# Kernel tuning notes

Hardware: AMD Instinct MI355X
Metric: run time of the kernel (lower is better)

The kernel has to match this reference:

```python
import jax, jax.numpy as jnp
import numpy as np

NUM_HEADS = 16
ROPE_BASE = 10000.0
QK_GAIN_INIT = 12.0
EPS = 1e-6
# head_config = alternating ['rope','nope',...]; 1.0 -> RoPE applied to this head
ROPE_MASK = jnp.asarray(np.tile([1.0, 0.0], NUM_HEADS // 2), dtype=jnp.float32)


def setup_inputs() -> dict:
    key = jax.random.key(0)
    k0, k1, k2 = jax.random.split(key, 3)
    B, S, Dm = 2, 2048, 2048
    x = jax.random.normal(k0, (B, S, Dm), dtype=jnp.float32)
    # fused QKV projection and output projection (out_proj flagged zero-init in the
    # original; we use small random init so outputs/grads are non-trivial)
    w_qkv = jax.random.normal(k1, (Dm, 3 * Dm), dtype=jnp.float32) * (Dm ** -0.5)
    w_out = jax.random.normal(k2, (Dm, Dm), dtype=jnp.float32) * (Dm ** -0.5)
    q_gain = jnp.full((NUM_HEADS,), QK_GAIN_INIT, dtype=jnp.float32)
    return {"x": x, "w_qkv": w_qkv, "w_out": w_out, "q_gain": q_gain}


def _rope_cos_sin(seqlen, head_dim, dtype):
    half = head_dim // 2
    inv_freq = ROPE_BASE ** (-jnp.arange(0, half, dtype=jnp.float32) / half)
    theta = jnp.arange(seqlen, dtype=jnp.float32)[:, None] * inv_freq[None, :]  # [S, D/2]
    return jnp.cos(theta).astype(dtype), jnp.sin(theta).astype(dtype)


def _apply_rope(t, cos, sin):
    # t: [B, S, H, D]; cos/sin: [S, D/2] -> broadcast [1, S, 1, D/2]
    d2 = t.shape[-1] // 2
    t1, t2 = t[..., :d2], t[..., d2:]
    c = cos[None, :, None, :]
    s = sin[None, :, None, :]
    return jnp.concatenate([t1 * c - t2 * s, t1 * s + t2 * c], axis=-1)


def _unit_norm(t):
    # per-head-dim L2 normalization (qk-norm)
    return t * jax.lax.rsqrt(jnp.sum(t * t, axis=-1, keepdims=True) + EPS)


def reference(x, w_qkv, w_out, q_gain):
    B, S, Dm = x.shape
    H = NUM_HEADS
    D = Dm // H
    qkv = (x @ w_qkv).reshape(B, S, 3, H, D)
    q, k, v = qkv[:, :, 0], qkv[:, :, 1], qkv[:, :, 2]  # [B, S, H, D]
    q = _unit_norm(q)
    k = _unit_norm(k)
    cos, sin = _rope_cos_sin(S, D, x.dtype)
    m = ROPE_MASK[None, None, :, None]  # heterogeneous per-head dispatch
    q = m * _apply_rope(q, cos, sin) + (1.0 - m) * q
    k = m * _apply_rope(k, cos, sin) + (1.0 - m) * k
    # per-head learned qk gain instead of 1/sqrt(d)
    logits = jnp.einsum('bshd,bthd->bhst', q, k) * q_gain[None, :, None, None]
    causal = jnp.tril(jnp.ones((S, S), dtype=bool))
    logits = jnp.where(causal[None, None], logits, jnp.finfo(logits.dtype).min)
    attn = jax.nn.softmax(logits, axis=-1)
    y = jnp.einsum('bhst,bthd->bshd', attn, v).reshape(B, S, Dm)
    return y @ w_out
```

## Files before the change

### kernel.cpp

```cpp
#include <hip/hip_runtime.h>
#include <hip/hip_bf16.h>

typedef unsigned short ushort_t;
typedef __attribute__((ext_vector_type(8))) short short8;
typedef __attribute__((ext_vector_type(4))) float floatx4;

#define B_  2
#define S_  2048
#define DM_ 2048
#define H_  16
#define DH_ 128

#define AS1(p) ((const __attribute__((address_space(1))) void*)(p))
#define AS3(p) ((__attribute__((address_space(3))) void*)(p))

static __device__ __forceinline__ float b2f(ushort_t u) {
  __hip_bfloat16 h = *reinterpret_cast<__hip_bfloat16*>(&u);
  return __bfloat162float(h);
}
static __device__ __forceinline__ ushort_t f2b(float f) {
  __hip_bfloat16 h = __float2bfloat16(f);
  return *reinterpret_cast<ushort_t*>(&h);
}

__global__ __launch_bounds__(256) void convert_f32_bf16(const float* __restrict__ in,
                                                        ushort_t* __restrict__ out) {
  size_t i = ((size_t)blockIdx.x * 256 + threadIdx.x) * 8;
  float4 a = *(const float4*)(in + i);
  float4 b = *(const float4*)(in + i + 4);
  ushort_t tmp[8] = {f2b(a.x), f2b(a.y), f2b(a.z), f2b(a.w),
                     f2b(b.x), f2b(b.y), f2b(b.z), f2b(b.w)};
  *(uint4*)(out + i) = *(const uint4*)tmp;
}

__global__ __launch_bounds__(256) void transpose_f32_to_bf16T(const float* __restrict__ in,
                                                              ushort_t* __restrict__ out,
                                                              int R, int inC, int colOff) {
  __shared__ ushort_t tile[64][72];
  const int tid = threadIdx.x;
  const int r0 = blockIdx.y * 64, c0 = blockIdx.x * 64;
#pragma unroll
  for (int p = 0; p < 2; ++p) {
    int li = tid + p * 256;
    int r = li >> 3, cs = (li & 7) * 8;
    const float* src = in + (size_t)(r0 + r) * inC + colOff + c0 + cs;
    float4 a = *(const float4*)src;
    float4 b = *(const float4*)(src + 4);
    ushort_t tmp[8] = {f2b(a.x), f2b(a.y), f2b(a.z), f2b(a.w),
                       f2b(b.x), f2b(b.y), f2b(b.z), f2b(b.w)};
    *(uint4*)&tile[r][cs] = *(const uint4*)tmp;
  }
  __syncthreads();
#pragma unroll
  for (int p = 0; p < 2; ++p) {
    int li = tid + p * 256;
    int cR = li >> 3, rs = (li & 7) * 8;
    ushort_t tmp[8];
#pragma unroll
    for (int e = 0; e < 8; ++e) tmp[e] = tile[rs + e][cR];
    *(uint4*)(out + (size_t)(c0 + cR) * R + r0 + rs) = *(const uint4*)tmp;
  }
}

template <int MODE>
__global__ __launch_bounds__(256) void gemm_bt_async(const ushort_t* __restrict__ A,
                                                     const ushort_t* __restrict__ Bt,
                                                     void* __restrict__ C0,
                                                     void* __restrict__ C1,
                                                     int M, int N, int K) {
  __shared__ alignas(16) ushort_t As[2][128 * 32];
  __shared__ alignas(16) ushort_t Bs[2][128 * 32];
  const int tid = threadIdx.x;
  const int wave = tid >> 6, lane = tid & 63;
  const int l15 = lane & 15, quad = lane >> 4;
  const int wr = (wave >> 1) * 64, wc = (wave & 1) * 64;
  const int lin = blockIdx.y * gridDim.x + blockIdx.x;
  const int band = lin / (4 * gridDim.x);
  const int rin = lin % (4 * gridDim.x);
  const int by = band * 4 + (rin & 3);
  const int bx = rin >> 2;
  const size_t m0 = (size_t)by * 128, n0 = (size_t)bx * 128;
  const int srow = lane >> 2, scol = (lane & 3) * 8;

  floatx4 zero = {0.f, 0.f, 0.f, 0.f};
  floatx4 acc[4][4];
#pragma unroll
  for (int i = 0; i < 4; ++i)
#pragma unroll
    for (int j = 0; j < 4; ++j) acc[i][j] = zero;

  auto stage = [&](int kt, int bf) {
#pragma unroll
    for (int i = 0; i < 2; ++i) {
      int c = wave * 2 + i;
      int row = c * 16 + srow;
      __builtin_amdgcn_global_load_lds(AS1(A + (m0 + row) * K + kt + scol),
                                       AS3((char*)As[bf] + c * 1024), 16, 0, 0);
      __builtin_amdgcn_global_load_lds(AS1(Bt + (n0 + row) * K + kt + scol),
                                       AS3((char*)Bs[bf] + c * 1024), 16, 0, 0);
    }
  };

  stage(0, 0);
  const int niter = K / 32;
  for (int it = 0; it < niter; ++it) {
    const int cur = it & 1;
    __syncthreads();
    if (it + 1 < niter) stage((it + 1) * 32, cur ^ 1);

    short8 af[4], bfr[4];
#pragma unroll
    for (int i = 0; i < 4; ++i)
      af[i] = *(const short8*)&As[cur][(wr + i * 16 + l15) * 32 + quad * 8];
#pragma unroll
    for (int j = 0; j < 4; ++j)
      bfr[j] = *(const short8*)&Bs[cur][(wc + j * 16 + l15) * 32 + quad * 8];
#pragma unroll
    for (int i = 0; i < 4; ++i)
#pragma unroll
      for (int j = 0; j < 4; ++j)
        acc[i][j] = __builtin_amdgcn_mfma_f32_16x16x32_bf16(af[i], bfr[j], acc[i][j], 0, 0, 0);
  }

  if (MODE == 2) {
    ushort_t* Cb = (n0 >= 2048) ? (ushort_t*)C1 : (ushort_t*)C0;
    size_t nc0 = n0 & 2047;
#pragma unroll
    for (int i = 0; i < 4; ++i)
#pragma unroll
      for (int j = 0; j < 4; ++j)
#pragma unroll
        for (int r = 0; r < 4; ++r) {
          size_t row = m0 + wr + i * 16 + quad * 4 + r;
          size_t col = nc0 + wc + j * 16 + l15;
          Cb[row * 2048 + col] = f2b(acc[i][j][r]);
        }
  } else {
#pragma unroll
    for (int i = 0; i < 4; ++i)
#pragma unroll
      for (int j = 0; j < 4; ++j)
#pragma unroll
        for (int r = 0; r < 4; ++r) {
          size_t row = m0 + wr + i * 16 + quad * 4 + r;
          size_t col = n0 + wc + j * 16 + l15;
          if (MODE == 1)
            ((float*)C0)[row * N + col] = acc[i][j][r];
          else
            ((ushort_t*)C0)[row * N + col] = f2b(acc[i][j][r]);
        }
  }
}

__global__ __launch_bounds__(256) void norm_rope(ushort_t* __restrict__ Q,
                                                 ushort_t* __restrict__ Kb,
                                                 const float* __restrict__ gain) {
  const int tid = threadIdx.x;
  const int wave = tid >> 6, lane = tid & 63;
  const int idx = blockIdx.x * 4 + wave;
  const int h = idx & 15;
  const int s = (idx >> 4) & (S_ - 1);
  const size_t off = (size_t)(idx >> 4) * DM_ + h * DH_;

  float q1 = b2f(Q[off + lane]),  q2 = b2f(Q[off + 64 + lane]);
  float k1 = b2f(Kb[off + lane]), k2 = b2f(Kb[off + 64 + lane]);

  float sq = q1 * q1 + q2 * q2;
  float sk = k1 * k1 + k2 * k2;
#pragma unroll
  for (int o = 1; o < 64; o <<= 1) {
    sq += __shfl_xor(sq, o, 64);
    sk += __shfl_xor(sk, o, 64);
  }
  float rq = rsqrtf(sq + 1e-6f), rk = rsqrtf(sk + 1e-6f);
  q1 *= rq; q2 *= rq; k1 *= rk; k2 *= rk;

  float qo1 = q1, qo2 = q2, ko1 = k1, ko2 = k2;
  if ((h & 1) == 0) {
    float invf = powf(10000.0f, -(float)lane * (1.0f / 64.0f));
    float th = (float)s * invf;
    float c = cosf(th), sn = sinf(th);
    qo1 = q1 * c - q2 * sn;  qo2 = q1 * sn + q2 * c;
    ko1 = k1 * c - k2 * sn;  ko2 = k1 * sn + k2 * c;
  }
  float g = gain[h];
  qo1 *= g; qo2 *= g;

  Q[off + lane]       = f2b(qo1);
  Q[off + 64 + lane]  = f2b(qo2);
  Kb[off + lane]      = f2b(ko1);
  Kb[off + 64 + lane] = f2b(ko2);
}

__global__ __launch_bounds__(256, 2) void attn(ushort_t* __restrict__ QY,
                                               const ushort_t* __restrict__ Kg,
                                               const ushort_t* __restrict__ Vg) {
  __shared__ alignas(16) ushort_t Ks[2][64 * 128];
  __shared__ alignas(16) ushort_t Vs[2][128 * 64];
  __shared__ alignas(16) ushort_t Ps[2][4][16 * 64];

  const float M0 = 13.0f;
  const int tid = threadIdx.x;
  const int wave = tid >> 6, lane = tid & 63;
  const int l15 = lane & 15, quad = lane >> 4;
  const int bh = blockIdx.y;
  const int b = bh >> 4, h = bh & 15;
  const int p = blockIdx.x;
  const int qt[2] = {p, 31 - p};

  const ushort_t* Kgb = Kg + (size_t)b * S_ * DM_ + h * DH_;
  const ushort_t* Vgb = Vg + (size_t)(h * DH_) * (B_ * S_) + b * S_;

  short8 aq[2][4];
#pragma unroll
  for (int t = 0; t < 2; ++t) {
    const ushort_t* Qg =
        QY + (size_t)(b * S_ + qt[t] * 64 + wave * 16 + l15) * DM_ + h * DH_;
#pragma unroll
    for (int ks = 0; ks < 4; ++ks)
      aq[t][ks] = *(const short8*)(Qg + ks * 32 + quad * 8);
  }

  float lsum[2][4] = {{0.f, 0.f, 0.f, 0.f}, {0.f, 0.f, 0.f, 0.f}};
  floatx4 zero = {0.f, 0.f, 0.f, 0.f};
  floatx4 oacc[2][8];
#pragma unroll
  for (int t = 0; t < 2; ++t)
#pragma unroll
    for (int d = 0; d < 8; ++d) oacc[t][d] = zero;

  const int krow_in = lane >> 4, ksd = lane & 15;
  const int vrow_in = lane >> 3, vsd = lane & 7;

  auto stage = [&](int kt, int bf) {
#pragma unroll
    for (int i = 0; i < 4; ++i) {
      int c = wave * 4 + i;
      {
        int r = c * 4 + krow_in;
        int sg = ksd ^ (r & 7);
        __builtin_amdgcn_global_load_lds(
            AS1(Kgb + (size_t)(kt * 64 + r) * DM_ + sg * 8),
            AS3((char*)Ks[bf] + c * 1024), 16, 0, 0);
      }
      {
        int r = c * 8 + vrow_in;
        int sg = vsd ^ (r & 7);
        __builtin_amdgcn_global_load_lds(
            AS1(Vgb + (size_t)r * (B_ * S_) + kt * 64 + sg * 8),
            AS3((char*)Vs[bf] + c * 1024), 16, 0, 0);
      }
    }
  };

  stage(0, 0);

  for (int kt = 0; kt <= qt[1]; ++kt) {
    const int cur = kt & 1;
    __syncthreads();
    if (kt < qt[1]) stage(kt + 1, cur ^ 1);

#pragma unroll
    for (int t = 0; t < 2; ++t) {
      if (t == 0 && kt > qt[0]) continue;
      floatx4 sacc[4];
#pragma unroll
      for (int j = 0; j < 4; ++j) sacc[j] = zero;
#pragma unroll
      for (int ks = 0; ks < 4; ++ks) {
#pragma unroll
        for (int j = 0; j < 4; ++j) {
          int row = j * 16 + l15;
          int sl = (ks * 4 + quad) ^ (row & 7);
          short8 bk = *(const short8*)&Ks[cur][row * 128 + sl * 8];
          sacc[j] = __builtin_amdgcn_mfma_f32_16x16x32_bf16(aq[t][ks], bk, sacc[j], 0, 0, 0);
        }
      }
      if (kt == qt[t]) {
#pragma unroll
        for (int j = 0; j < 4; ++j)
#pragma unroll
          for (int r = 0; r < 4; ++r) {
            int key = j * 16 + l15;
            int qr = wave * 16 + quad * 4 + r;
            if (key > qr) sacc[j][r] = -1e30f;
          }
      }
#pragma unroll
      for (int j = 0; j < 4; ++j)
#pragma unroll
        for (int r = 0; r < 4; ++r) {
          float pv = __expf(sacc[j][r] - M0);
          sacc[j][r] = pv;
          lsum[t][r] += pv;
        }
#pragma unroll
      for (int j = 0; j < 4; ++j)
#pragma unroll
        for (int r = 0; r < 4; ++r) {
          int row = quad * 4 + r;
          int col = j * 16 + l15;
          int g = col >> 3, w = col & 7;
          Ps[t][wave][row * 64 + ((g ^ (row & 7)) << 3) + w] = f2b(sacc[j][r]);
        }
#pragma unroll
      for (int ks2 = 0; ks2 < 2; ++ks2) {
        short8 ap = *(const short8*)&Ps[t][wave][l15 * 64 +
                                                (((ks2 * 4 + quad) ^ (l15 & 7)) << 3)];
#pragma unroll
        for (int d = 0; d < 8; ++d) {
          int row = d * 16 + l15;
          int sl = (ks2 * 4 + quad) ^ (row & 7);
          short8 bv = *(const short8*)&Vs[cur][row * 64 + sl * 8];
          oacc[t][d] = __builtin_amdgcn_mfma_f32_16x16x32_bf16(ap, bv, oacc[t][d], 0, 0, 0);
        }
      }
    }
  }

#pragma unroll
  for (int t = 0; t < 2; ++t) {
#pragma unroll
    for (int r = 0; r < 4; ++r) {
#pragma unroll
      for (int o = 1; o < 16; o <<= 1) lsum[t][r] += __shfl_xor(lsum[t][r], o, 64);
      float inv = 1.0f / lsum[t][r];
      size_t row = (size_t)(b * S_ + qt[t] * 64 + wave * 16 + quad * 4 + r);
#pragma unroll
      for (int d = 0; d < 8; ++d) {
        size_t col = (size_t)h * DH_ + d * 16 + l15;
        QY[row * DM_ + col] = f2b(oacc[t][d][r] * inv);
      }
    }
  }
}

extern "C" void kernel_launch(void* const* d_in, const int* in_sizes, int n_in,
                              void* d_out, int out_size, void* d_ws, size_t ws_size,
                              hipStream_t stream) {
  const float* x      = (const float*)d_in[0];
  const float* w_qkv  = (const float*)d_in[1];
  const float* w_out  = (const float*)d_in[2];
  const float* q_gain = (const float*)d_in[3];
  float* out = (float*)d_out;

  char* ws = (char*)d_ws;
  const size_t bsd = (size_t)B_ * S_ * DM_;
  ushort_t* Qraw = (ushort_t*)ws;
  ushort_t* Kraw = Qraw + bsd;
  ushort_t* Vt   = Kraw + bsd;
  ushort_t* wvT  = Vt + bsd;
  ushort_t* xbf  = (ushort_t*)d_out;
  ushort_t* wqkT = xbf + bsd;
  ushort_t* woutT = Kraw;

  convert_f32_bf16<<<dim3(bsd / (8 * 256)), 256, 0, stream>>>(x, xbf);
  transpose_f32_to_bf16T<<<dim3(64, 32), 256, 0, stream>>>(w_qkv, wqkT, DM_, 3 * DM_, 0);
  transpose_f32_to_bf16T<<<dim3(32, 32), 256, 0, stream>>>(w_qkv, wvT, DM_, 3 * DM_, 2 * DM_);

  gemm_bt_async<2><<<dim3(32, 32), 256, 0, stream>>>(xbf, wqkT, Qraw, Kraw,
                                                     B_ * S_, 2 * DM_, DM_);
  gemm_bt_async<0><<<dim3(32, 16), 256, 0, stream>>>(wvT, xbf, Vt, nullptr,
                                                     DM_, B_ * S_, DM_);
  norm_rope<<<dim3(B_ * S_ * H_ / 4), 256, 0, stream>>>(Qraw, Kraw, q_gain);
  attn<<<dim3(S_ / 128, B_ * H_), 256, 0, stream>>>(Qraw, Kraw, Vt);
  transpose_f32_to_bf16T<<<dim3(32, 32), 256, 0, stream>>>(w_out, woutT, DM_, DM_, 0);
  gemm_bt_async<1><<<dim3(16, 32), 256, 0, stream>>>(Qraw, woutT, out, nullptr,
                                                     B_ * S_, DM_, DM_);
}
```

Measured before the change: 420.1 us.

## Add 256x256-tile pipelined GEMM kernel for the fused QK projection

Adds a new GEMM kernel with 512 threads, a 256x256 output tile, a K-step of 64 and swizzled LDS. Loads are staged in quarter-tiles interleaved with four MFMA quadrants, using sched barriers, setprio and explicit vmcnt waits. The QK projection now uses it in place of the 128x128 async GEMM. The aim is more operand reuse per byte loaded and overlap of global-to-LDS copies with MFMA. In exchange it uses 128KB of LDS and many accumulator registers, and launches only 256 blocks.

```diff
diff --git a/kernel.cpp b/kernel.cpp
--- a/kernel.cpp
+++ b/kernel.cpp
@@ -122,32 +122,172 @@
         acc[i][j] = __builtin_amdgcn_mfma_f32_16x16x32_bf16(af[i], bfr[j], acc[i][j], 0, 0, 0);
   }
 
+#pragma unroll
+  for (int i = 0; i < 4; ++i)
+#pragma unroll
+    for (int j = 0; j < 4; ++j)
+#pragma unroll
+      for (int r = 0; r < 4; ++r) {
+        size_t row = m0 + wr + i * 16 + quad * 4 + r;
+        size_t col = n0 + wc + j * 16 + l15;
+        if (MODE == 1)
+          ((float*)C0)[row * N + col] = acc[i][j][r];
+        else
+          ((ushort_t*)C0)[row * N + col] = f2b(acc[i][j][r]);
+      }
+}
+
+#define SBAR() __builtin_amdgcn_sched_barrier(0)
+#define BARR() __builtin_amdgcn_s_barrier()
+
+#define LDS_A(qm, bb)                                                          \
+  _Pragma("unroll") for (int mi = 0; mi < 4; ++mi) {                           \
+    _Pragma("unroll") for (int ks = 0; ks < 2; ++ks) {                         \
+      const int r_ = arow + (qm) * 64 + mi * 16;                               \
+      const int cb_ = ((ks) * 64 + quad * 16) ^ swz;                           \
+      afr[qm][mi][ks] =                                                        \
+          *(const short8*)((const char*)As[bb] + r_ * 128 + cb_);              \
+    }                                                                          \
+  }
+
+#define LDS_B(qn, bb)                                                          \
+  _Pragma("unroll") for (int ni = 0; ni < 2; ++ni) {                           \
+    _Pragma("unroll") for (int ks = 0; ks < 2; ++ks) {                         \
+      const int r_ = brow + (qn) * 32 + ni * 16;                               \
+      const int cb_ = ((ks) * 64 + quad * 16) ^ swz;                           \
+      bfr[qn][ni][ks] =                                                        \
+          *(const short8*)((const char*)Bs[bb] + r_ * 128 + cb_);              \
+    }                                                                          \
+  }
+
+#define MMA_Q(qm, qn)                                                          \
+  _Pragma("unroll") for (int mi = 0; mi < 4; ++mi) {                           \
+    _Pragma("unroll") for (int ni = 0; ni < 2; ++ni) {                         \
+      floatx4 t_ = acc[(qm) * 4 + mi][(qn) * 2 + ni];                          \
+      t_ = __builtin_amdgcn_mfma_f32_16x16x32_bf16(afr[qm][mi][0],             \
+                                                   bfr[qn][ni][0], t_, 0, 0, 0); \
+      t_ = __builtin_amdgcn_mfma_f32_16x16x32_bf16(afr[qm][mi][1],             \
+                                                   bfr[qn][ni][1], t_, 0, 0, 0); \
+      acc[(qm) * 4 + mi][(qn) * 2 + ni] = t_;                                  \
+    }                                                                          \
+  }
+
+template <int MODE>
+__global__ __launch_bounds__(512, 2) void gemm_bt_256(const ushort_t* __restrict__ A,
+                                                      const ushort_t* __restrict__ Bt,
+                                                      void* __restrict__ C0,
+                                                      void* __restrict__ C1,
+                                                      int M, int N, int K) {
+  __shared__ alignas(16) ushort_t As[2][256 * 64];
+  __shared__ alignas(16) ushort_t Bs[2][256 * 64];
+  const int tid = threadIdx.x;
+  const int wave = tid >> 6, lane = tid & 63;
+  const int l15 = lane & 15, quad = lane >> 4;
+  const int wm = wave >> 2, wn = wave & 3;
+  const size_t m0 = (size_t)blockIdx.y * 256, n0 = (size_t)blockIdx.x * 256;
+  const int nkt = K >> 6;
+
+  const int srow = lane >> 3;
+  const int skk = ((lane & 7) ^ srow) * 8;
+
+  const int arow = wm * 128 + l15;
+  const int brow = wn * 64 + l15;
+  const int swz = (l15 & 7) << 4;
+
+  floatx4 zero = {0.f, 0.f, 0.f, 0.f};
+  floatx4 acc[8][4];
+#pragma unroll
+  for (int i = 0; i < 8; ++i)
+#pragma unroll
+    for (int j = 0; j < 4; ++j) acc[i][j] = zero;
+
+  short8 afr[2][4][2];
+  short8 bfr[2][2][2];
+
+  auto stage_half = [&](int t, int ht) {
+    if (t >= nkt) return;
+    const int bb = t & 1;
+    const int h = ht & 1;
+    const int kt64 = t << 6;
+    const ushort_t* G = (ht < 2) ? A : Bt;
+    const size_t r0 = (ht < 2) ? m0 : n0;
+    char* dst = (char*)((ht < 2) ? As[bb] : Bs[bb]) + h * 16384;
+#pragma unroll
+    for (int i = 0; i < 2; ++i) {
+      const int c = wave * 2 + i;
+      const size_t gr = r0 + h * 128 + c * 8 + srow;
+      __builtin_amdgcn_global_load_lds(AS1(G + gr * K + kt64 + skk),
+                                       AS3(dst + c * 1024), 16, 0, 0);
+    }
+  };
+
+  stage_half(0, 0); stage_half(0, 1); stage_half(0, 2); stage_half(0, 3);
+  stage_half(1, 0); stage_half(1, 1);
+  SBAR();
+  if (nkt > 1) { asm volatile("s_waitcnt vmcnt(4)" ::: "memory"); }
+  else         { asm volatile("s_waitcnt vmcnt(0)" ::: "memory"); }
+  SBAR(); BARR(); SBAR();
+
+  for (int kt = 0; kt < nkt; ++kt) {
+    const int bb = kt & 1;
+    LDS_A(0, bb); LDS_B(0, bb);
+    stage_half(kt + 1, 2);
+    SBAR(); BARR(); SBAR();
+    __builtin_amdgcn_s_setprio(1);
+    MMA_Q(0, 0);
+    __builtin_amdgcn_s_setprio(0);
+    SBAR(); BARR(); SBAR();
+    LDS_A(1, bb);
+    stage_half(kt + 1, 3);
+    SBAR(); BARR(); SBAR();
+    __builtin_amdgcn_s_setprio(1);
+    MMA_Q(1, 0);
+    __builtin_amdgcn_s_setprio(0);
+    SBAR(); BARR(); SBAR();
+    LDS_B(1, bb);
+    stage_half(kt + 2, 0);
+    SBAR(); BARR(); SBAR();
+    __builtin_amdgcn_s_setprio(1);
+    MMA_Q(1, 1);
+    __builtin_amdgcn_s_setprio(0);
+    SBAR(); BARR(); SBAR();
+    stage_half(kt + 2, 1);
+    SBAR(); BARR(); SBAR();
+    __builtin_amdgcn_s_setprio(1);
+    MMA_Q(0, 1);
+    __builtin_amdgcn_s_setprio(0);
+    SBAR();
+    if (kt + 2 < nkt) { asm volatile("s_waitcnt vmcnt(4)" ::: "memory"); }
+    else              { asm volatile("s_waitcnt vmcnt(0)" ::: "memory"); }
+    SBAR(); BARR(); SBAR();
+  }
+
   if (MODE == 2) {
     ushort_t* Cb = (n0 >= 2048) ? (ushort_t*)C1 : (ushort_t*)C0;
     size_t nc0 = n0 & 2047;
 #pragma unroll
-    for (int i = 0; i < 4; ++i)
-#pragma unroll
-      for (int j = 0; j < 4; ++j)
+    for (int mi8 = 0; mi8 < 8; ++mi8)
+#pragma unroll
+      for (int nj = 0; nj < 4; ++nj)
 #pragma unroll
         for (int r = 0; r < 4; ++r) {
-          size_t row = m0 + wr + i * 16 + quad * 4 + r;
-          size_t col = nc0 + wc + j * 16 + l15;
-          Cb[row * 2048 + col] = f2b(acc[i][j][r]);
+          size_t row = m0 + wm * 128 + (mi8 >> 2) * 64 + (mi8 & 3) * 16 + quad * 4 + r;
+          size_t col = nc0 + wn * 64 + (nj >> 1) * 32 + (nj & 1) * 16 + l15;
+          Cb[row * 2048 + col] = f2b(acc[mi8][nj][r]);
         }
   } else {
 #pragma unroll
-    for (int i = 0; i < 4; ++i)
-#pragma unroll
-      for (int j = 0; j < 4; ++j)
+    for (int mi8 = 0; mi8 < 8; ++mi8)
+#pragma unroll
+      for (int nj = 0; nj < 4; ++nj)
 #pragma unroll
         for (int r = 0; r < 4; ++r) {
-          size_t row = m0 + wr + i * 16 + quad * 4 + r;
-          size_t col = n0 + wc + j * 16 + l15;
+          size_t row = m0 + wm * 128 + (mi8 >> 2) * 64 + (mi8 & 3) * 16 + quad * 4 + r;
+          size_t col = n0 + wn * 64 + (nj >> 1) * 32 + (nj & 1) * 16 + l15;
           if (MODE == 1)
-            ((float*)C0)[row * N + col] = acc[i][j][r];
+            ((float*)C0)[row * N + col] = acc[mi8][nj][r];
           else
-            ((ushort_t*)C0)[row * N + col] = f2b(acc[i][j][r]);
+            ((ushort_t*)C0)[row * N + col] = f2b(acc[mi8][nj][r]);
         }
   }
 }
@@ -358,8 +498,8 @@
   transpose_f32_to_bf16T<<<dim3(64, 32), 256, 0, stream>>>(w_qkv, wqkT, DM_, 3 * DM_, 0);
   transpose_f32_to_bf16T<<<dim3(32, 32), 256, 0, stream>>>(w_qkv, wvT, DM_, 3 * DM_, 2 * DM_);
 
-  gemm_bt_async<2><<<dim3(32, 32), 256, 0, stream>>>(xbf, wqkT, Qraw, Kraw,
-                                                     B_ * S_, 2 * DM_, DM_);
+  gemm_bt_256<2><<<dim3(16, 16), 512, 0, stream>>>(xbf, wqkT, Qraw, Kraw,
+                                                   B_ * S_, 2 * DM_, DM_);
   gemm_bt_async<0><<<dim3(32, 16), 256, 0, stream>>>(wvT, xbf, Vt, nullptr,
                                                      DM_, B_ * S_, DM_);
   norm_rope<<<dim3(B_ * S_ * H_ / 4), 256, 0, stream>>>(Qraw, Kraw, q_gain);
```

New measurement: 392.4 us. 6.6% less time.
